# Kernel optimization log

Hardware: AMD Instinct MI355X
Metric: run time of the kernel (lower is better)

## Reference

```python
import jax, jax.numpy as jnp
import numpy as np

N, C, K = 100000, 64, 27
EPS = 1e-5


def setup_inputs() -> dict:
    key = jax.random.key(0)
    ks = jax.random.split(key, 8)
    feats = jax.random.normal(ks[0], (N, C), dtype=jnp.float32)
    W1 = jax.random.normal(ks[1], (K, C, C), dtype=jnp.float32) * (1.0 / np.sqrt(K * C))
    W2 = jax.random.normal(ks[2], (K, C, C), dtype=jnp.float32) * (1.0 / np.sqrt(K * C))
    gamma1 = jnp.ones((C,), dtype=jnp.float32)
    beta1 = jnp.zeros((C,), dtype=jnp.float32)
    gamma2 = jnp.ones((C,), dtype=jnp.float32)
    beta2 = jnp.zeros((C,), dtype=jnp.float32)
    nbr_idx1 = jax.random.randint(ks[3], (K, N), 0, N, dtype=jnp.int32)
    nbr_idx2 = jax.random.randint(ks[4], (K, N), 0, N, dtype=jnp.int32)
    nbr_mask1 = (jax.random.uniform(ks[5], (K, N)) < 0.7).astype(jnp.float32)
    nbr_mask2 = (jax.random.uniform(ks[6], (K, N)) < 0.7).astype(jnp.float32)
    return {"feats": feats, "W1": W1, "gamma1": gamma1, "beta1": beta1,
            "W2": W2, "gamma2": gamma2, "beta2": beta2,
            "nbr_idx1": nbr_idx1, "nbr_mask1": nbr_mask1,
            "nbr_idx2": nbr_idx2, "nbr_mask2": nbr_mask2}


def sparse_conv(f, idx, mask, W):
    # gather per kernel offset: [K, N, C], mask out missing neighbors
    g = f[idx] * mask[..., None]
    # per-offset GEMM and accumulate over offsets -> [N, C_out]
    return jnp.einsum('knc,kcd->nd', g, W)


def batch_norm(x, gamma, beta):
    # MinkowskiBatchNorm (training): stats over all N points, per channel
    mean = jnp.mean(x, axis=0)
    var = jnp.mean(jnp.square(x - mean), axis=0)
    return (x - mean) * jax.lax.rsqrt(var + EPS) * gamma + beta


def reference(feats, W1, gamma1, beta1, W2, gamma2, beta2,
              nbr_idx1, nbr_mask1, nbr_idx2, nbr_mask2):
    out = sparse_conv(feats, nbr_idx1, nbr_mask1, W1)
    out = jax.nn.relu(batch_norm(out, gamma1, beta1))
    out = sparse_conv(out, nbr_idx2, nbr_mask2, W2)
    out = batch_norm(out, gamma2, beta2)
    out = out + feats          # identity residual (stride=1, no downsample)
    return jax.nn.relu(out)
```

## Files before the change

kernel.cpp:

```cpp
#include <hip/hip_runtime.h>
#include <hip/hip_bf16.h>
#include <stdint.h>
#include <stddef.h>

#define N_PTS 100000
#define KOFF 27

typedef __attribute__((ext_vector_type(8))) __bf16 bf16x8;
typedef __attribute__((ext_vector_type(16))) float f32x16;

__device__ inline unsigned short f2bf(float f) {
  union { float f; unsigned u; } x; x.f = f;
  unsigned r = x.u + 0x7fffu + ((x.u >> 16) & 1u);
  return (unsigned short)(r >> 16);
}

__global__ void prep_kernel(const float* __restrict__ feats,
                            const float* __restrict__ W1,
                            const float* __restrict__ W2,
                            unsigned short* __restrict__ featsb,
                            unsigned short* __restrict__ wf1,
                            unsigned short* __restrict__ wf2,
                            float* __restrict__ stats) {
  int tid = blockIdx.x * blockDim.x + threadIdx.x;
  int stride = gridDim.x * blockDim.x;
  const int NF4 = N_PTS * 64 / 4;
  for (int i = tid; i < NF4; i += stride) {
    float4 v = ((const float4*)feats)[i];
    ushort4 o;
    o.x = f2bf(v.x); o.y = f2bf(v.y); o.z = f2bf(v.z); o.w = f2bf(v.w);
    ((ushort4*)featsb)[i] = o;
  }
  const int WTOT = KOFF * 4096;
  for (int i = tid; i < 2 * WTOT; i += stride) {
    int which = (i >= WTOT) ? 1 : 0;
    int o = which ? (i - WTOT) : i;
    int j = o & 7, l = (o >> 3) & 63, ct = (o >> 9) & 1, ks = (o >> 10) & 3, k = o >> 12;
    int c = ks * 16 + ((l >> 5) << 3) + j;
    int d = (ct << 5) + (l & 31);
    const float* W = which ? W2 : W1;
    float val = W[k * 4096 + c * 64 + d];
    (which ? wf2 : wf1)[o] = f2bf(val);
  }
  for (int i = tid; i < 256; i += stride) stats[i] = 0.f;
}

__global__ __launch_bounds__(256) void conv_kernel(
    const unsigned short* __restrict__ fin,
    const unsigned short* __restrict__ wf,
    const int* __restrict__ idx,
    const float* __restrict__ mask,
    float* __restrict__ yout,
    float* __restrict__ gsum,
    float* __restrict__ gsq)
{
  int lane = threadIdx.x & 63;
  int wid  = threadIdx.x >> 6;
  int col  = lane & 31;
  int hi   = lane >> 5;
  int n0   = blockIdx.x * 128 + wid * 32;
  int n    = n0 + col;
  bool valid = n < N_PTS;

  f32x16 acc0, acc1;
#pragma unroll
  for (int r = 0; r < 16; ++r) { acc0[r] = 0.f; acc1[r] = 0.f; }

  const uint4* wfv = (const uint4*)wf;

  for (int k = 0; k < KOFF; ++k) {
    int gi = 0; float m = 0.f;
    if (valid) {
      gi = idx[k * N_PTS + n];
      m  = mask[k * N_PTS + n];
    }
    const uint4* arow = (const uint4*)(fin + (size_t)gi * 64);
    uint4 a0 = arow[hi];
    uint4 a1 = arow[2 + hi];
    uint4 a2 = arow[4 + hi];
    uint4 a3 = arow[6 + hi];
    if (m == 0.f) {
      a0 = make_uint4(0u, 0u, 0u, 0u); a1 = a0; a2 = a0; a3 = a0;
    }
    const uint4* bp = wfv + (size_t)k * 512 + lane;
    uint4 b00 = bp[0];   uint4 b01 = bp[64];
    uint4 b10 = bp[128]; uint4 b11 = bp[192];
    uint4 b20 = bp[256]; uint4 b21 = bp[320];
    uint4 b30 = bp[384]; uint4 b31 = bp[448];

    acc0 = __builtin_amdgcn_mfma_f32_32x32x16_bf16(__builtin_bit_cast(bf16x8, a0), __builtin_bit_cast(bf16x8, b00), acc0, 0, 0, 0);
    acc1 = __builtin_amdgcn_mfma_f32_32x32x16_bf16(__builtin_bit_cast(bf16x8, a0), __builtin_bit_cast(bf16x8, b01), acc1, 0, 0, 0);
    acc0 = __builtin_amdgcn_mfma_f32_32x32x16_bf16(__builtin_bit_cast(bf16x8, a1), __builtin_bit_cast(bf16x8, b10), acc0, 0, 0, 0);
    acc1 = __builtin_amdgcn_mfma_f32_32x32x16_bf16(__builtin_bit_cast(bf16x8, a1), __builtin_bit_cast(bf16x8, b11), acc1, 0, 0, 0);
    acc0 = __builtin_amdgcn_mfma_f32_32x32x16_bf16(__builtin_bit_cast(bf16x8, a2), __builtin_bit_cast(bf16x8, b20), acc0, 0, 0, 0);
    acc1 = __builtin_amdgcn_mfma_f32_32x32x16_bf16(__builtin_bit_cast(bf16x8, a2), __builtin_bit_cast(bf16x8, b21), acc1, 0, 0, 0);
    acc0 = __builtin_amdgcn_mfma_f32_32x32x16_bf16(__builtin_bit_cast(bf16x8, a3), __builtin_bit_cast(bf16x8, b30), acc0, 0, 0, 0);
    acc1 = __builtin_amdgcn_mfma_f32_32x32x16_bf16(__builtin_bit_cast(bf16x8, a3), __builtin_bit_cast(bf16x8, b31), acc1, 0, 0, 0);
  }

  __shared__ float s_sum[64], s_sq[64];
  if (threadIdx.x < 64) { s_sum[threadIdx.x] = 0.f; s_sq[threadIdx.x] = 0.f; }
  __syncthreads();

  float s0 = 0.f, q0 = 0.f, s1 = 0.f, q1 = 0.f;
#pragma unroll
  for (int r = 0; r < 16; ++r) {
    float v = acc0[r]; s0 += v; q0 += v * v;
    float w = acc1[r]; s1 += w; q1 += w * w;
    int rr = (r & 3) + ((r >> 2) << 3) + (hi << 2);
    int nr = n0 + rr;
    if (nr < N_PTS) {
      yout[(size_t)nr * 64 + col]      = v;
      yout[(size_t)nr * 64 + 32 + col] = w;
    }
  }
  atomicAdd(&s_sum[col], s0);
  atomicAdd(&s_sq[col],  q0);
  atomicAdd(&s_sum[32 + col], s1);
  atomicAdd(&s_sq[32 + col],  q1);
  __syncthreads();
  if (threadIdx.x < 64) {
    atomicAdd(&gsum[threadIdx.x], s_sum[threadIdx.x]);
    atomicAdd(&gsq[threadIdx.x],  s_sq[threadIdx.x]);
  }
}

__global__ void bn1_kernel(const float* __restrict__ y,
                           const float* __restrict__ sum,
                           const float* __restrict__ sq,
                           const float* __restrict__ gamma,
                           const float* __restrict__ beta,
                           unsigned short* __restrict__ outb) {
  __shared__ float s_scale[64], s_shift[64];
  if (threadIdx.x < 64) {
    int c = threadIdx.x;
    float mean = sum[c] * (1.f / N_PTS);
    float var  = sq[c] * (1.f / N_PTS) - mean * mean;
    float inv  = rsqrtf(var + 1e-5f);
    float sc   = gamma[c] * inv;
    s_scale[c] = sc;
    s_shift[c] = beta[c] - mean * sc;
  }
  __syncthreads();
  int tid = blockIdx.x * blockDim.x + threadIdx.x;
  int stride = gridDim.x * blockDim.x;
  const int NT = N_PTS * 64 / 4;
  for (int i = tid; i < NT; i += stride) {
    float4 v = ((const float4*)y)[i];
    int c = (i * 4) & 63;
    float r0 = fmaxf(v.x * s_scale[c]     + s_shift[c],     0.f);
    float r1 = fmaxf(v.y * s_scale[c + 1] + s_shift[c + 1], 0.f);
    float r2 = fmaxf(v.z * s_scale[c + 2] + s_shift[c + 2], 0.f);
    float r3 = fmaxf(v.w * s_scale[c + 3] + s_shift[c + 3], 0.f);
    ushort4 o;
    o.x = f2bf(r0); o.y = f2bf(r1); o.z = f2bf(r2); o.w = f2bf(r3);
    ((ushort4*)outb)[i] = o;
  }
}

__global__ void bn2_kernel(const float* __restrict__ y,
                           const float* __restrict__ sum,
                           const float* __restrict__ sq,
                           const float* __restrict__ gamma,
                           const float* __restrict__ beta,
                           const float* __restrict__ feats,
                           float* __restrict__ out) {
  __shared__ float s_scale[64], s_shift[64];
  if (threadIdx.x < 64) {
    int c = threadIdx.x;
    float mean = sum[c] * (1.f / N_PTS);
    float var  = sq[c] * (1.f / N_PTS) - mean * mean;
    float inv  = rsqrtf(var + 1e-5f);
    float sc   = gamma[c] * inv;
    s_scale[c] = sc;
    s_shift[c] = beta[c] - mean * sc;
  }
  __syncthreads();
  int tid = blockIdx.x * blockDim.x + threadIdx.x;
  int stride = gridDim.x * blockDim.x;
  const int NT = N_PTS * 64 / 4;
  for (int i = tid; i < NT; i += stride) {
    float4 v = ((const float4*)y)[i];
    float4 f = ((const float4*)feats)[i];
    int c = (i * 4) & 63;
    float4 o;
    o.x = fmaxf(v.x * s_scale[c]     + s_shift[c]     + f.x, 0.f);
    o.y = fmaxf(v.y * s_scale[c + 1] + s_shift[c + 1] + f.y, 0.f);
    o.z = fmaxf(v.z * s_scale[c + 2] + s_shift[c + 2] + f.z, 0.f);
    o.w = fmaxf(v.w * s_scale[c + 3] + s_shift[c + 3] + f.w, 0.f);
    ((float4*)out)[i] = o;
  }
}

extern "C" void kernel_launch(void* const* d_in, const int* in_sizes, int n_in,
                              void* d_out, int out_size, void* d_ws, size_t ws_size,
                              hipStream_t stream) {
  const float* feats  = (const float*)d_in[0];
  const float* W1     = (const float*)d_in[1];
  const float* gamma1 = (const float*)d_in[2];
  const float* beta1  = (const float*)d_in[3];
  const float* W2     = (const float*)d_in[4];
  const float* gamma2 = (const float*)d_in[5];
  const float* beta2  = (const float*)d_in[6];
  const int*   idx1   = (const int*)d_in[7];
  const float* mask1  = (const float*)d_in[8];
  const int*   idx2   = (const int*)d_in[9];
  const float* mask2  = (const float*)d_in[10];
  float* out = (float*)d_out;

  char* ws = (char*)d_ws;
  unsigned short* featsb = (unsigned short*)(ws + 0);
  unsigned short* wf1    = (unsigned short*)(ws + 12800000);
  unsigned short* wf2    = (unsigned short*)(ws + 13021184);
  float*          stats  = (float*)(ws + 13242368);
  unsigned short* f2b    = (unsigned short*)(ws + 13243392);

  float* sum1 = stats;       float* sq1 = stats + 64;
  float* sum2 = stats + 128; float* sq2 = stats + 192;

  float* y = out;

  prep_kernel<<<1024, 256, 0, stream>>>(feats, W1, W2, featsb, wf1, wf2, stats);

  const int CONV_GRID = (N_PTS + 127) / 128;
  conv_kernel<<<CONV_GRID, 256, 0, stream>>>(featsb, wf1, idx1, mask1, y, sum1, sq1);
  bn1_kernel<<<1024, 256, 0, stream>>>(y, sum1, sq1, gamma1, beta1, f2b);
  conv_kernel<<<CONV_GRID, 256, 0, stream>>>(f2b, wf2, idx2, mask2, y, sum2, sq2);
  bn2_kernel<<<1024, 256, 0, stream>>>(y, sum2, sq2, gamma2, beta2, feats, out);
}
```

Measured before the change: 357.0 us.

## Software-pipeline conv gathers with double-buffered A/B registers and zero-row masking

The conv loop is restructured so that the gather of the next offset's features and weights, plus the index and mask loads two offsets ahead, are issued before the current offset's MFMAs. This hides gather latency behind compute. Masked neighbors are redirected to an appended zero row in the bf16 feature buffers, which removes the select after the load. Weight repacking moves to a separate kernel that stages each offset's weights through shared memory for coalesced reads, and launch bounds request 3 waves per SIMD. The risk is higher register pressure from the double buffers, which could lower occupancy.

```diff
diff --git a/kernel.cpp b/kernel.cpp
--- a/kernel.cpp
+++ b/kernel.cpp
@@ -15,37 +15,85 @@
   return (unsigned short)(r >> 16);
 }
 
-__global__ void prep_kernel(const float* __restrict__ feats,
-                            const float* __restrict__ W1,
-                            const float* __restrict__ W2,
-                            unsigned short* __restrict__ featsb,
-                            unsigned short* __restrict__ wf1,
-                            unsigned short* __restrict__ wf2,
-                            float* __restrict__ stats) {
+__global__ void fprep_kernel(const float* __restrict__ feats,
+                             unsigned short* __restrict__ featsb,
+                             unsigned short* __restrict__ f2b,
+                             float* __restrict__ stats) {
   int tid = blockIdx.x * blockDim.x + threadIdx.x;
   int stride = gridDim.x * blockDim.x;
-  const int NF4 = N_PTS * 64 / 4;
+  const int NF4 = N_PTS * 16;
   for (int i = tid; i < NF4; i += stride) {
     float4 v = ((const float4*)feats)[i];
     ushort4 o;
     o.x = f2bf(v.x); o.y = f2bf(v.y); o.z = f2bf(v.z); o.w = f2bf(v.w);
     ((ushort4*)featsb)[i] = o;
   }
-  const int WTOT = KOFF * 4096;
-  for (int i = tid; i < 2 * WTOT; i += stride) {
-    int which = (i >= WTOT) ? 1 : 0;
-    int o = which ? (i - WTOT) : i;
-    int j = o & 7, l = (o >> 3) & 63, ct = (o >> 9) & 1, ks = (o >> 10) & 3, k = o >> 12;
+  if (tid < 256) stats[tid] = 0.f;
+  if (tid >= 256 && tid < 264) {
+    uint4 z = make_uint4(0u, 0u, 0u, 0u);
+    ((uint4*)(featsb + (size_t)N_PTS * 64))[tid - 256] = z;
+  }
+  if (tid >= 264 && tid < 272) {
+    uint4 z = make_uint4(0u, 0u, 0u, 0u);
+    ((uint4*)(f2b + (size_t)N_PTS * 64))[tid - 264] = z;
+  }
+}
+
+__global__ __launch_bounds__(256) void wprep_kernel(const float* __restrict__ W1,
+                                                    const float* __restrict__ W2,
+                                                    unsigned short* __restrict__ wf1,
+                                                    unsigned short* __restrict__ wf2) {
+  __shared__ float sW[4096];
+  int which = blockIdx.x & 1;
+  int k = blockIdx.x >> 1;
+  const float* W = (which ? W2 : W1) + (size_t)k * 4096;
+  unsigned short* wf = (which ? wf2 : wf1) + (size_t)k * 4096;
+  int t = threadIdx.x;
+#pragma unroll
+  for (int i = 0; i < 4; ++i) {
+    ((float4*)sW)[t + 256 * i] = ((const float4*)W)[t + 256 * i];
+  }
+  __syncthreads();
+#pragma unroll
+  for (int i = 0; i < 16; ++i) {
+    int o = i * 256 + t;
+    int j = o & 7, l = (o >> 3) & 63, ct = (o >> 9) & 1, ks = o >> 10;
     int c = ks * 16 + ((l >> 5) << 3) + j;
     int d = (ct << 5) + (l & 31);
-    const float* W = which ? W2 : W1;
-    float val = W[k * 4096 + c * 64 + d];
-    (which ? wf2 : wf1)[o] = f2bf(val);
-  }
-  for (int i = tid; i < 256; i += stride) stats[i] = 0.f;
-}
-
-__global__ __launch_bounds__(256) void conv_kernel(
+    wf[o] = f2bf(sW[c * 64 + d]);
+  }
+}
+
+#define MFMA(a, b, c) __builtin_amdgcn_mfma_f32_32x32x16_bf16(__builtin_bit_cast(bf16x8, a), __builtin_bit_cast(bf16x8, b), c, 0, 0, 0)
+
+#define STEP(Ac, Bc, An, Bn, giN, mN, giF, mF, kcur)                         \
+  {                                                                          \
+    int gie = (mN != 0.f) ? giN : N_PTS;                                     \
+    const uint4* ar = (const uint4*)(fin + (size_t)gie * 64);                \
+    An[0] = ar[hi]; An[1] = ar[2 + hi]; An[2] = ar[4 + hi]; An[3] = ar[6 + hi]; \
+    {                                                                        \
+      int kn = ((kcur) + 1 <= 26) ? (kcur) + 1 : 26;                         \
+      const uint4* bp = wfv + (size_t)kn * 512 + lane;                       \
+      Bn[0] = bp[0];   Bn[1] = bp[64];  Bn[2] = bp[128]; Bn[3] = bp[192];    \
+      Bn[4] = bp[256]; Bn[5] = bp[320]; Bn[6] = bp[384]; Bn[7] = bp[448];    \
+    }                                                                        \
+    {                                                                        \
+      int kf = ((kcur) + 2 <= 26) ? (kcur) + 2 : 26;                         \
+      giF = idxp[kf * N_PTS];                                                \
+      float mt = mp[kf * N_PTS];                                             \
+      mF = valid ? mt : 0.f;                                                 \
+    }                                                                        \
+    acc0 = MFMA(Ac[0], Bc[0], acc0);                                         \
+    acc1 = MFMA(Ac[0], Bc[1], acc1);                                         \
+    acc0 = MFMA(Ac[1], Bc[2], acc0);                                         \
+    acc1 = MFMA(Ac[1], Bc[3], acc1);                                         \
+    acc0 = MFMA(Ac[2], Bc[4], acc0);                                         \
+    acc1 = MFMA(Ac[2], Bc[5], acc1);                                         \
+    acc0 = MFMA(Ac[3], Bc[6], acc0);                                         \
+    acc1 = MFMA(Ac[3], Bc[7], acc1);                                         \
+  }
+
+__global__ __launch_bounds__(256, 3) void conv_kernel(
     const unsigned short* __restrict__ fin,
     const unsigned short* __restrict__ wf,
     const int* __restrict__ idx,
@@ -61,42 +109,45 @@
   int n0   = blockIdx.x * 128 + wid * 32;
   int n    = n0 + col;
   bool valid = n < N_PTS;
+  int nc = valid ? n : (N_PTS - 1);
+
+  const int*   idxp = idx + nc;
+  const float* mp   = mask + nc;
+  const uint4* wfv  = (const uint4*)wf;
 
   f32x16 acc0, acc1;
 #pragma unroll
   for (int r = 0; r < 16; ++r) { acc0[r] = 0.f; acc1[r] = 0.f; }
 
-  const uint4* wfv = (const uint4*)wf;
-
-  for (int k = 0; k < KOFF; ++k) {
-    int gi = 0; float m = 0.f;
-    if (valid) {
-      gi = idx[k * N_PTS + n];
-      m  = mask[k * N_PTS + n];
-    }
-    const uint4* arow = (const uint4*)(fin + (size_t)gi * 64);
-    uint4 a0 = arow[hi];
-    uint4 a1 = arow[2 + hi];
-    uint4 a2 = arow[4 + hi];
-    uint4 a3 = arow[6 + hi];
-    if (m == 0.f) {
-      a0 = make_uint4(0u, 0u, 0u, 0u); a1 = a0; a2 = a0; a3 = a0;
-    }
-    const uint4* bp = wfv + (size_t)k * 512 + lane;
-    uint4 b00 = bp[0];   uint4 b01 = bp[64];
-    uint4 b10 = bp[128]; uint4 b11 = bp[192];
-    uint4 b20 = bp[256]; uint4 b21 = bp[320];
-    uint4 b30 = bp[384]; uint4 b31 = bp[448];
-
-    acc0 = __builtin_amdgcn_mfma_f32_32x32x16_bf16(__builtin_bit_cast(bf16x8, a0), __builtin_bit_cast(bf16x8, b00), acc0, 0, 0, 0);
-    acc1 = __builtin_amdgcn_mfma_f32_32x32x16_bf16(__builtin_bit_cast(bf16x8, a0), __builtin_bit_cast(bf16x8, b01), acc1, 0, 0, 0);
-    acc0 = __builtin_amdgcn_mfma_f32_32x32x16_bf16(__builtin_bit_cast(bf16x8, a1), __builtin_bit_cast(bf16x8, b10), acc0, 0, 0, 0);
-    acc1 = __builtin_amdgcn_mfma_f32_32x32x16_bf16(__builtin_bit_cast(bf16x8, a1), __builtin_bit_cast(bf16x8, b11), acc1, 0, 0, 0);
-    acc0 = __builtin_amdgcn_mfma_f32_32x32x16_bf16(__builtin_bit_cast(bf16x8, a2), __builtin_bit_cast(bf16x8, b20), acc0, 0, 0, 0);
-    acc1 = __builtin_amdgcn_mfma_f32_32x32x16_bf16(__builtin_bit_cast(bf16x8, a2), __builtin_bit_cast(bf16x8, b21), acc1, 0, 0, 0);
-    acc0 = __builtin_amdgcn_mfma_f32_32x32x16_bf16(__builtin_bit_cast(bf16x8, a3), __builtin_bit_cast(bf16x8, b30), acc0, 0, 0, 0);
-    acc1 = __builtin_amdgcn_mfma_f32_32x32x16_bf16(__builtin_bit_cast(bf16x8, a3), __builtin_bit_cast(bf16x8, b31), acc1, 0, 0, 0);
-  }
+  uint4 A0[4], A1[4], B0[8], B1[8];
+  int gi0, gi1; float m0, m1;
+
+  gi0 = idxp[0];
+  { float mt = mp[0]; m0 = valid ? mt : 0.f; }
+  {
+    int gie = (m0 != 0.f) ? gi0 : N_PTS;
+    const uint4* ar = (const uint4*)(fin + (size_t)gie * 64);
+    A0[0] = ar[hi]; A0[1] = ar[2 + hi]; A0[2] = ar[4 + hi]; A0[3] = ar[6 + hi];
+    const uint4* bp = wfv + lane;
+    B0[0] = bp[0];   B0[1] = bp[64];  B0[2] = bp[128]; B0[3] = bp[192];
+    B0[4] = bp[256]; B0[5] = bp[320]; B0[6] = bp[384]; B0[7] = bp[448];
+  }
+  gi1 = idxp[N_PTS];
+  { float mt = mp[N_PTS]; m1 = valid ? mt : 0.f; }
+
+  for (int kk = 0; kk < 13; ++kk) {
+    int k = 2 * kk;
+    STEP(A0, B0, A1, B1, gi1, m1, gi0, m0, k);
+    STEP(A1, B1, A0, B0, gi0, m0, gi1, m1, k + 1);
+  }
+  acc0 = MFMA(A0[0], B0[0], acc0);
+  acc1 = MFMA(A0[0], B0[1], acc1);
+  acc0 = MFMA(A0[1], B0[2], acc0);
+  acc1 = MFMA(A0[1], B0[3], acc1);
+  acc0 = MFMA(A0[2], B0[4], acc0);
+  acc1 = MFMA(A0[2], B0[5], acc1);
+  acc0 = MFMA(A0[3], B0[6], acc0);
+  acc1 = MFMA(A0[3], B0[7], acc1);
 
   __shared__ float s_sum[64], s_sq[64];
   if (threadIdx.x < 64) { s_sum[threadIdx.x] = 0.f; s_sq[threadIdx.x] = 0.f; }
@@ -144,7 +195,7 @@
   __syncthreads();
   int tid = blockIdx.x * blockDim.x + threadIdx.x;
   int stride = gridDim.x * blockDim.x;
-  const int NT = N_PTS * 64 / 4;
+  const int NT = N_PTS * 16;
   for (int i = tid; i < NT; i += stride) {
     float4 v = ((const float4*)y)[i];
     int c = (i * 4) & 63;
@@ -178,7 +229,7 @@
   __syncthreads();
   int tid = blockIdx.x * blockDim.x + threadIdx.x;
   int stride = gridDim.x * blockDim.x;
-  const int NT = N_PTS * 64 / 4;
+  const int NT = N_PTS * 16;
   for (int i = tid; i < NT; i += stride) {
     float4 v = ((const float4*)y)[i];
     float4 f = ((const float4*)feats)[i];
@@ -210,17 +261,18 @@
 
   char* ws = (char*)d_ws;
   unsigned short* featsb = (unsigned short*)(ws + 0);
-  unsigned short* wf1    = (unsigned short*)(ws + 12800000);
-  unsigned short* wf2    = (unsigned short*)(ws + 13021184);
-  float*          stats  = (float*)(ws + 13242368);
-  unsigned short* f2b    = (unsigned short*)(ws + 13243392);
+  unsigned short* wf1    = (unsigned short*)(ws + 12800768);
+  unsigned short* wf2    = (unsigned short*)(ws + 13021952);
+  float*          stats  = (float*)(ws + 13243136);
+  unsigned short* f2b    = (unsigned short*)(ws + 13244160);
 
   float* sum1 = stats;       float* sq1 = stats + 64;
   float* sum2 = stats + 128; float* sq2 = stats + 192;
 
   float* y = out;
 
-  prep_kernel<<<1024, 256, 0, stream>>>(feats, W1, W2, featsb, wf1, wf2, stats);
+  fprep_kernel<<<1024, 256, 0, stream>>>(feats, featsb, f2b, stats);
+  wprep_kernel<<<54, 256, 0, stream>>>(W1, W2, wf1, wf2);
 
   const int CONV_GRID = (N_PTS + 127) / 128;
   conv_kernel<<<CONV_GRID, 256, 0, stream>>>(featsb, wf1, idx1, mask1, y, sum1, sq1);
```

Measured after the change: 335.1 us. -6.1%, faster.
